# Kernel optimization log

Measured on AMD Instinct MI355X. Metric: run time of the kernel, lower is better.

The kernel has to match this reference:

```python
import jax, jax.numpy as jnp
import numpy as np

B, C, T, F = 4, 96, 320, 256
BN_EPS = 1e-5


def _cbp(x, W, b, gamma, beta, mean, var, a):
    """1x1 Conv2d + BatchNorm2d (inference stats) + PReLU (single param)."""
    y = jnp.einsum('oc,bctf->botf', W, x) + b[None, :, None, None]
    scale = gamma * jax.lax.rsqrt(var + BN_EPS)
    y = (y - mean[None, :, None, None]) * scale[None, :, None, None] + beta[None, :, None, None]
    return jnp.where(y >= 0, y, a * y)


def setup_inputs() -> dict:
    key = jax.random.key(0)
    ks = jax.random.split(key, 24)
    d = {"inp": jax.random.normal(ks[0], (B, C, T, F), dtype=jnp.float32)}

    def mk_params(i, cout):
        kk = jax.random.split(ks[i], 7)
        return dict(
            W=jax.random.normal(kk[0], (cout, C), dtype=jnp.float32) / np.sqrt(C),
            b=jnp.zeros((cout,), dtype=jnp.float32),
            gamma=jnp.ones((cout,), dtype=jnp.float32) + 0.1 * jax.random.normal(kk[1], (cout,), dtype=jnp.float32),
            beta=0.1 * jax.random.normal(kk[2], (cout,), dtype=jnp.float32),
            mean=0.1 * jax.random.normal(kk[3], (cout,), dtype=jnp.float32),
            var=jax.random.uniform(kk[4], (cout,), dtype=jnp.float32) + 0.5,
            a=jnp.float32(0.25),
        )

    for tag, i, cout in (("f", 1, 3 * C), ("t", 2, 2 * C), ("p", 3, C)):
        p = mk_params(i, cout)
        for k, v in p.items():
            d[k + "_" + tag] = v
    return d


def reference(inp,
              W_f, b_f, gamma_f, beta_f, mean_f, var_f, a_f,
              W_t, b_t, gamma_t, beta_t, mean_t, var_t, a_t,
              W_p, b_p, gamma_p, beta_p, mean_p, var_p, a_p):
    c = inp.shape[1]
    scale = 1.0 / jnp.sqrt(jnp.float32(c))

    # frequency-axis attention
    f_qkv = _cbp(inp, W_f, b_f, gamma_f, beta_f, mean_f, var_f, a_f)  # [B,3C,T,F]
    qf, kf, v = f_qkv[:, :c], f_qkv[:, c:2 * c], f_qkv[:, 2 * c:]
    f_score = jnp.einsum('bctf,bcty->btfy', qf, kf) * scale
    f_score = jax.nn.softmax(f_score, axis=-1)
    f_out = jnp.einsum('btfy,bcty->bctf', f_score, v)

    # time-axis attention (NOTE: original's masked_fill is non-inplace and
    # its result is discarded, so the causal mask has NO effect; replicated.)
    t_qk = _cbp(inp, W_t, b_t, gamma_t, beta_t, mean_t, var_t, a_t)  # [B,2C,T,F]
    qt, kt = t_qk[:, :c], t_qk[:, c:]
    t_score = jnp.einsum('bctf,bcyf->bfty', qt, kt) * scale
    t_score = jax.nn.softmax(t_score, axis=-1)
    t_out = jnp.einsum('bfty,bcyf->bctf', t_score, f_out)

    out = _cbp(t_out, W_p, b_p, gamma_p, beta_p, mean_p, var_p, a_p)
    return out + inp
```

## Files before the change

kernel.cpp:

```cpp
#include <hip/hip_runtime.h>
#include <math.h>

typedef float f4 __attribute__((ext_vector_type(4)));
typedef float f2 __attribute__((ext_vector_type(2)));
typedef float f32x4 __attribute__((ext_vector_type(4)));
typedef _Float16 h8 __attribute__((ext_vector_type(8)));

constexpr int B_ = 4, C_ = 96, T_ = 320, F_ = 256;
constexpr int TF_ = T_ * F_;
constexpr float EPS_ = 1e-5f;
constexpr size_t QH_ = (size_t)C_ * TF_;

constexpr int WHF = 0, WLF = 27648, WHT = 55296, WLT = 73728,
              WHP = 92160, WLP = 101376, WTOT = 110592;

__global__ __launch_bounds__(256)
void prep_kernel(const float* __restrict__ Wf, const float* __restrict__ Wt,
                 const float* __restrict__ Wp,
                 const float* __restrict__ bf, const float* __restrict__ gf,
                 const float* __restrict__ bef, const float* __restrict__ mf,
                 const float* __restrict__ vf,
                 const float* __restrict__ bt, const float* __restrict__ gt,
                 const float* __restrict__ bet, const float* __restrict__ mt,
                 const float* __restrict__ vt,
                 const float* __restrict__ bp, const float* __restrict__ gp,
                 const float* __restrict__ bep, const float* __restrict__ mp,
                 const float* __restrict__ vp,
                 _Float16* __restrict__ wsp, float* __restrict__ scsh)
{
    const int gtid = blockIdx.x * 256 + threadIdx.x;
    const int gsz  = gridDim.x * 256;
    for (int i = gtid; i < 27648; i += gsz) {
        const float w = Wf[i]; const _Float16 h = (_Float16)w;
        wsp[WHF + i] = h; wsp[WLF + i] = (_Float16)(w - (float)h);
    }
    for (int i = gtid; i < 18432; i += gsz) {
        const float w = Wt[i]; const _Float16 h = (_Float16)w;
        wsp[WHT + i] = h; wsp[WLT + i] = (_Float16)(w - (float)h);
    }
    for (int i = gtid; i < 9216; i += gsz) {
        const float w = Wp[i]; const _Float16 h = (_Float16)w;
        wsp[WHP + i] = h; wsp[WLP + i] = (_Float16)(w - (float)h);
    }
    if (gtid < 288) {
        const float sc = gf[gtid] * rsqrtf(vf[gtid] + EPS_);
        scsh[2 * gtid] = sc;
        scsh[2 * gtid + 1] = fmaf(bf[gtid] - mf[gtid], sc, bef[gtid]);
    } else if (gtid < 480) {
        const int i = gtid - 288;
        const float sc = gt[i] * rsqrtf(vt[i] + EPS_);
        scsh[576 + 2 * i] = sc;
        scsh[576 + 2 * i + 1] = fmaf(bt[i] - mt[i], sc, bet[i]);
    } else if (gtid < 576) {
        const int i = gtid - 480;
        const float sc = gp[i] * rsqrtf(vp[i] + EPS_);
        scsh[960 + 2 * i] = sc;
        scsh[960 + 2 * i + 1] = fmaf(bp[i] - mp[i], sc, bep[i]);
    }
}

__global__ __launch_bounds__(256, 3)
void conv_ft(const float* __restrict__ x, const _Float16* __restrict__ wsp,
             const float* __restrict__ scsh,
             const float* __restrict__ aPf, const float* __restrict__ aPt,
             _Float16* __restrict__ yf, _Float16* __restrict__ yt,
             int bsx, int bsyf, int bsyt)
{
    constexpr int LS = 200;
    extern __shared__ _Float16 ldsh[];
    _Float16* Xs = ldsh;

    x  += (size_t)blockIdx.y * bsx;
    yf += (size_t)blockIdx.y * bsyf;
    yt += (size_t)blockIdx.y * bsyt;

    const int tid = threadIdx.x;
    const int p0  = blockIdx.x * 64;

    const float* xg = x + p0;
    for (int e = tid; e < 64 * 12; e += 256) {
        const int p = e & 63, k0 = (e >> 6) * 8;
        const float* xp = xg + (size_t)k0 * TF_ + p;
        h8 hv, lv;
#pragma unroll
        for (int j = 0; j < 8; ++j) {
            const float xv = xp[(size_t)j * TF_];
            const _Float16 xh = (_Float16)xv;
            hv[j] = xh;
            lv[j] = (_Float16)(xv - (float)xh);
        }
        *(h8*)&Xs[p * LS + k0]      = hv;
        *(h8*)&Xs[p * LS + 96 + k0] = lv;
    }

    const int lane = tid & 63, wid = tid >> 6;
    const int l16 = lane & 15, lg = lane >> 4;
    const int wm = wid >> 1, wn = wid & 1;
    const float af_ = aPf[0], at_ = aPt[0];
    __syncthreads();

#pragma unroll 1
    for (int cg = 0; cg < 5; ++cg) {
        const _Float16 *Wh, *Wl; const float* ss; float a; _Float16* yo;
        if (cg < 3) {
            Wh = wsp + WHF + cg * 9216;  Wl = wsp + WLF + cg * 9216;
            ss = scsh + cg * 192;        a = af_;
            yo = yf + (size_t)cg * QH_;
        } else {
            const int c2 = cg - 3;
            Wh = wsp + WHT + c2 * 9216;  Wl = wsp + WLT + c2 * 9216;
            ss = scsh + 576 + c2 * 192;  a = at_;
            yo = yt + (size_t)c2 * QH_;
        }

        f32x4 acc[3][2];
#pragma unroll
        for (int m = 0; m < 3; ++m)
#pragma unroll
            for (int n = 0; n < 2; ++n) acc[m][n] = (f32x4){0.f, 0.f, 0.f, 0.f};

#pragma unroll
        for (int kk = 0; kk < 3; ++kk) {
            h8 bfh[2], bfl[2];
#pragma unroll
            for (int n = 0; n < 2; ++n) {
                const int prow = (wn * 2 + n) * 16 + l16;
                bfh[n] = *(const h8*)&Xs[prow * LS + kk * 32 + lg * 8];
                bfl[n] = *(const h8*)&Xs[prow * LS + 96 + kk * 32 + lg * 8];
            }
#pragma unroll
            for (int m = 0; m < 3; ++m) {
                const int row = (wm * 3 + m) * 16 + l16;
                const h8 wh = *(const h8*)&Wh[row * 96 + kk * 32 + lg * 8];
                const h8 wl = *(const h8*)&Wl[row * 96 + kk * 32 + lg * 8];
#pragma unroll
                for (int n = 0; n < 2; ++n) {
                    acc[m][n] = __builtin_amdgcn_mfma_f32_16x16x32_f16(wh, bfh[n], acc[m][n], 0, 0, 0);
                    acc[m][n] = __builtin_amdgcn_mfma_f32_16x16x32_f16(wl, bfh[n], acc[m][n], 0, 0, 0);
                    acc[m][n] = __builtin_amdgcn_mfma_f32_16x16x32_f16(wh, bfl[n], acc[m][n], 0, 0, 0);
                }
            }
        }

#pragma unroll
        for (int m = 0; m < 3; ++m) {
#pragma unroll
            for (int r = 0; r < 4; ++r) {
                const int col = (wm * 3 + m) * 16 + lg * 4 + r;
                const f2 sp = *(const f2*)&ss[2 * col];
                _Float16* yr = yo + (size_t)col * TF_ + p0 + wn * 32 + l16;
#pragma unroll
                for (int n = 0; n < 2; ++n) {
                    const float v = fmaf(acc[m][n][r], sp[0], sp[1]);
                    yr[n * 16] = (_Float16)(v >= 0.f ? v : a * v);
                }
            }
        }
    }
}

__global__ __launch_bounds__(256, 3)
void conv_p(const _Float16* __restrict__ x, const _Float16* __restrict__ wsp,
            const float* __restrict__ scsh, const float* __restrict__ aPp,
            _Float16* __restrict__ y, int bsx, int bsy)
{
    constexpr int LS = 104, PT = 160, NN = 5;
    extern __shared__ _Float16 ldsh[];
    _Float16* Xs = ldsh;

    x += (size_t)blockIdx.y * bsx;
    y += (size_t)blockIdx.y * bsy;

    const int tid = threadIdx.x;
    const int pt  = blockIdx.x & 1;
    const int g   = blockIdx.x >> 1;
    const int p0  = pt * PT;

    const _Float16* xg = x + (size_t)g * 96 * T_ + p0;
    for (int e = tid; e < PT * 12; e += 256) {
        const int p = e % PT, k0 = (e / PT) * 8;
        const _Float16* xp = xg + (size_t)k0 * T_ + p;
        h8 hv;
#pragma unroll
        for (int j = 0; j < 8; ++j) hv[j] = xp[(size_t)j * T_];
        *(h8*)&Xs[p * LS + k0] = hv;
    }

    const int lane = tid & 63, wid = tid >> 6;
    const int l16 = lane & 15, lg = lane >> 4;
    const int wm = wid >> 1, wn = wid & 1;
    const float a = aPp[0];
    const _Float16* Wh = wsp + WHP;
    const _Float16* Wl = wsp + WLP;
    const float* ss = scsh + 960;
    __syncthreads();

    f32x4 acc[3][NN];
#pragma unroll
    for (int m = 0; m < 3; ++m)
#pragma unroll
        for (int n = 0; n < NN; ++n) acc[m][n] = (f32x4){0.f, 0.f, 0.f, 0.f};

#pragma unroll
    for (int kk = 0; kk < 3; ++kk) {
        h8 bf[NN];
#pragma unroll
        for (int n = 0; n < NN; ++n)
            bf[n] = *(const h8*)&Xs[((wn * NN + n) * 16 + l16) * LS + kk * 32 + lg * 8];
#pragma unroll
        for (int m = 0; m < 3; ++m) {
            const int row = (wm * 3 + m) * 16 + l16;
            const h8 wh = *(const h8*)&Wh[row * 96 + kk * 32 + lg * 8];
            const h8 wl = *(const h8*)&Wl[row * 96 + kk * 32 + lg * 8];
#pragma unroll
            for (int n = 0; n < NN; ++n) {
                acc[m][n] = __builtin_amdgcn_mfma_f32_16x16x32_f16(wh, bf[n], acc[m][n], 0, 0, 0);
                acc[m][n] = __builtin_amdgcn_mfma_f32_16x16x32_f16(wl, bf[n], acc[m][n], 0, 0, 0);
            }
        }
    }

#pragma unroll
    for (int m = 0; m < 3; ++m) {
#pragma unroll
        for (int r = 0; r < 4; ++r) {
            const int col = (wm * 3 + m) * 16 + lg * 4 + r;
            const f2 sp = *(const f2*)&ss[2 * col];
            _Float16* yr = y + ((size_t)g * 96 + col) * T_ + p0 + wn * NN * 16 + l16;
#pragma unroll
            for (int n = 0; n < NN; ++n) {
                const float v = fmaf(acc[m][n][r], sp[0], sp[1]);
                yr[n * 16] = (_Float16)(v >= 0.f ? v : a * v);
            }
        }
    }
}

__device__ __forceinline__ void tr64_body(const _Float16* __restrict__ in,
                                          _Float16* __restrict__ out,
                                          int Mo, int No, int n0, int m0,
                                          _Float16* tile)
{
    const int t = threadIdx.x, ty = t >> 3, tx8 = t & 7;
#pragma unroll
    for (int r = 0; r < 2; ++r) {
        const int n = ty + r * 32;
        const h8 v = *(const h8*)&in[(size_t)(n0 + n) * Mo + m0 + tx8 * 8];
        const int c = tx8 ^ (n >> 3);
        *(h8*)&tile[n * 72 + c * 8] = v;
    }
    __syncthreads();
#pragma unroll
    for (int r = 0; r < 2; ++r) {
        const int mt = ty + r * 32;
        h8 v;
#pragma unroll
        for (int j = 0; j < 8; ++j) {
            const int n = tx8 * 8 + j;
            const int c = (mt >> 3) ^ tx8;
            v[j] = tile[n * 72 + c * 8 + (mt & 7)];
        }
        *(h8*)&out[(size_t)(m0 + mt) * No + n0 + tx8 * 8] = v;
    }
}

__global__ __launch_bounds__(256)
void transpose_trA(const _Float16* __restrict__ doh, _Float16* __restrict__ wsh)
{
    __shared__ _Float16 tile[64 * 72];
    const int b = blockIdx.z >> 1, t = blockIdx.z & 1;
    const _Float16* in  = t ? doh + (size_t)b * 2 * QH_
                            : wsh + (size_t)b * 3 * QH_;
    _Float16*       out = t ? wsh + (size_t)b * 3 * QH_ + 2 * QH_
                            : wsh + (size_t)b * 3 * QH_ + QH_;
    tr64_body(in, out, F_, C_ * T_, blockIdx.x * 64, blockIdx.y * 64, tile);
}

__global__ __launch_bounds__(256)
void transpose_trB(const _Float16* __restrict__ doh, _Float16* __restrict__ wsh)
{
    __shared__ _Float16 tile[64 * 72];
    const int b = blockIdx.z;
    tr64_body(doh + (size_t)b * 2 * QH_ + QH_, wsh + (size_t)b * 3 * QH_,
              F_, C_ * T_, blockIdx.x * 64, blockIdx.y * 64, tile);
}

__global__ __launch_bounds__(256)
void transpose_hf_res(const _Float16* __restrict__ in, const float* __restrict__ res,
                      float* __restrict__ out, int si, int sr, int so)
{
    __shared__ _Float16 tile[64 * 72];
    in  += (size_t)blockIdx.z * si;
    res += (size_t)blockIdx.z * sr;
    out += (size_t)blockIdx.z * so;
    const int n0 = blockIdx.x * 64, m0 = blockIdx.y * 64;
    const int t = threadIdx.x, ty = t >> 3, tx8 = t & 7;
#pragma unroll
    for (int r = 0; r < 2; ++r) {
        const int n = ty + r * 32;
        const h8 v = *(const h8*)&in[(size_t)(n0 + n) * (C_ * T_) + m0 + tx8 * 8];
        const int c = tx8 ^ (n >> 3);
        *(h8*)&tile[n * 72 + c * 8] = v;
    }
    __syncthreads();
#pragma unroll
    for (int r = 0; r < 2; ++r) {
        const int mt = ty + r * 32;
        const size_t obase = (size_t)(m0 + mt) * F_ + n0 + tx8 * 8;
        const f4 r0 = *(const f4*)&res[obase];
        const f4 r1 = *(const f4*)&res[obase + 4];
        f4 o0, o1;
#pragma unroll
        for (int j = 0; j < 8; ++j) {
            const int n = tx8 * 8 + j;
            const int c = (mt >> 3) ^ tx8;
            const float v = (float)tile[n * 72 + c * 8 + (mt & 7)];
            if (j < 4) o0[j] = v + r0[j]; else o1[j - 4] = v + r1[j - 4];
        }
        *(f4*)&out[obase]     = o0;
        *(f4*)&out[obase + 4] = o1;
    }
}

template<int MODE>
__global__ __launch_bounds__(256, 2)
void attn_mfma(const _Float16* __restrict__ Qb, const _Float16* __restrict__ Kb,
               const _Float16* __restrict__ Vb, _Float16* __restrict__ Ob,
               int qs, int ks, int vs, int os)
{
    constexpr int NY  = (MODE == 0) ? 256 : 320;
    constexpr int LD  = (MODE == 0) ? TF_ : T_;
    constexpr int NT  = NY / 16;
    constexpr int NYK = NY / 32;
    constexpr int KS  = 104;
    constexpr int VPS = NY + 24;
    constexpr int KVH = (NY * KS > 96 * VPS) ? NY * KS : 96 * VPS;
    constexpr int NG  = (MODE == 0) ? T_ : F_;
    constexpr int GOFF = (MODE == 0) ? F_ : C_ * T_;

    extern __shared__ _Float16 ldsh[];
    _Float16* KV = ldsh;
    _Float16* Pw = ldsh + KVH;

    const int lb    = blockIdx.y;
    const int strip = blockIdx.x / NG;
    const int grp   = blockIdx.x % NG;
    const int m0    = strip * 64;
    const size_t off = (size_t)grp * GOFF;
    const _Float16* Q = Qb + (size_t)lb * qs + off;
    const _Float16* K = Kb + (size_t)lb * ks + off;
    const _Float16* V = Vb + (size_t)lb * vs + off;
    _Float16*       O = Ob + (size_t)lb * os + off;

    const int tid  = threadIdx.x;
    const int lane = tid & 63, wid = tid >> 6;
    const int l16  = lane & 15, lg = lane >> 4;
    const int mw   = wid * 16;
    const float scale = 0.10206207261596575f;

    for (int e = tid; e < NY * 12; e += 256) {
        const int yy = e % NY, k0 = (e / NY) * 8;
        const _Float16* kp = K + (size_t)k0 * LD + yy;
        h8 hv;
#pragma unroll
        for (int j = 0; j < 8; ++j) hv[j] = kp[(size_t)j * LD];
        *(h8*)&KV[yy * KS + k0] = hv;
    }

    h8 aQ[3];
#pragma unroll
    for (int kk = 0; kk < 3; ++kk) {
        const _Float16* qp = Q + (size_t)(kk * 32 + lg * 8) * LD + m0 + mw + l16;
#pragma unroll
        for (int j = 0; j < 8; ++j) aQ[kk][j] = qp[(size_t)j * LD];
    }
    __syncthreads();

    f32x4 sacc[NT];
#pragma unroll
    for (int t = 0; t < NT; ++t) sacc[t] = (f32x4){0.f, 0.f, 0.f, 0.f};
#pragma unroll
    for (int kk = 0; kk < 3; ++kk) {
#pragma unroll
        for (int t = 0; t < NT; ++t) {
            const h8 bK = *(const h8*)&KV[(t * 16 + l16) * KS + kk * 32 + lg * 8];
            sacc[t] = __builtin_amdgcn_mfma_f32_16x16x32_f16(aQ[kk], bK, sacc[t], 0, 0, 0);
        }
    }

#pragma unroll
    for (int r = 0; r < 4; ++r) {
        float mx = sacc[0][r];
#pragma unroll
        for (int t = 1; t < NT; ++t) mx = fmaxf(mx, sacc[t][r]);
        for (int d = 1; d < 16; d <<= 1) mx = fmaxf(mx, __shfl_xor(mx, d));
        float pv[NT];
        float sum = 0.f;
#pragma unroll
        for (int t = 0; t < NT; ++t) {
            pv[t] = __expf((sacc[t][r] - mx) * scale); sum += pv[t];
        }
        for (int d = 1; d < 16; d <<= 1) sum += __shfl_xor(sum, d);
        const float inv = 1.f / sum;
#pragma unroll
        for (int t = 0; t < NT; ++t) sacc[t][r] = pv[t] * inv;
    }
    __syncthreads();

    constexpr int NY8 = NY / 8;
    for (int e = tid; e < 96 * NY8; e += 256) {
        const int c = e / NY8, y8 = e - c * NY8;
        *(h8*)&KV[c * VPS + y8 * 8] = *(const h8*)(V + (size_t)c * LD + y8 * 8);
    }
    __syncthreads();

    _Float16* Pme = Pw + wid * 640;
    f32x4 oacc[6];
#pragma unroll
    for (int ct = 0; ct < 6; ++ct) oacc[ct] = (f32x4){0.f, 0.f, 0.f, 0.f};

#pragma unroll
    for (int yk = 0; yk < NYK; ++yk) {
#pragma unroll
        for (int h = 0; h < 2; ++h)
#pragma unroll
            for (int r = 0; r < 4; ++r)
                Pme[(lg * 4 + r) * 40 + h * 16 + l16] = (_Float16)sacc[2 * yk + h][r];
        const h8 pf = *(const h8*)&Pme[l16 * 40 + lg * 8];
#pragma unroll
        for (int ct = 0; ct < 6; ++ct) {
            const h8 av = *(const h8*)&KV[(ct * 16 + l16) * VPS + yk * 32 + lg * 8];
            oacc[ct] = __builtin_amdgcn_mfma_f32_16x16x32_f16(av, pf, oacc[ct], 0, 0, 0);
        }
    }
#pragma unroll
    for (int ct = 0; ct < 6; ++ct)
#pragma unroll
        for (int r = 0; r < 4; ++r)
            O[(size_t)(ct * 16 + lg * 4 + r) * LD + m0 + mw + l16] = (_Float16)oacc[ct][r];
}

extern "C" void kernel_launch(void* const* d_in, const int* in_sizes, int n_in,
                              void* d_out, int out_size, void* d_ws, size_t ws_size,
                              hipStream_t stream)
{
    const float* inp = (const float*)d_in[0];
    const float* W_f = (const float*)d_in[1];  const float* b_f = (const float*)d_in[2];
    const float* g_f = (const float*)d_in[3];  const float* be_f = (const float*)d_in[4];
    const float* m_f = (const float*)d_in[5];  const float* v_f = (const float*)d_in[6];
    const float* a_f = (const float*)d_in[7];
    const float* W_t = (const float*)d_in[8];  const float* b_t = (const float*)d_in[9];
    const float* g_t = (const float*)d_in[10]; const float* be_t = (const float*)d_in[11];
    const float* m_t = (const float*)d_in[12]; const float* v_t = (const float*)d_in[13];
    const float* a_t = (const float*)d_in[14];
    const float* W_p = (const float*)d_in[15]; const float* b_p = (const float*)d_in[16];
    const float* g_p = (const float*)d_in[17]; const float* be_p = (const float*)d_in[18];
    const float* m_p = (const float*)d_in[19]; const float* v_p = (const float*)d_in[20];
    const float* a_p = (const float*)d_in[21];

    hipFuncSetAttribute((const void*)conv_ft,
                        hipFuncAttributeMaxDynamicSharedMemorySize, 25600);
    hipFuncSetAttribute((const void*)conv_p,
                        hipFuncAttributeMaxDynamicSharedMemorySize, 33280);
    hipFuncSetAttribute((const void*)attn_mfma<0>,
                        hipFuncAttributeMaxDynamicSharedMemorySize, 58880);
    hipFuncSetAttribute((const void*)attn_mfma<1>,
                        hipFuncAttributeMaxDynamicSharedMemorySize, 71680);

    constexpr int QH = (int)QH_;
    const size_t need4 = (size_t)12 * QH * 2 + (size_t)WTOT * 2 + 1152 * 4 + 4096;
    const int G = (ws_size >= need4) ? 4 : 2;

    _Float16* wsh  = (_Float16*)d_ws;
    _Float16* wsp  = wsh + (size_t)3 * G * QH;
    float*    scsh = (float*)(wsp + WTOT);

    prep_kernel<<<dim3(128), dim3(256), 0, stream>>>(
        W_f, W_t, W_p, b_f, g_f, be_f, m_f, v_f,
        b_t, g_t, be_t, m_t, v_t, b_p, g_p, be_p, m_p, v_p, wsp, scsh);

    for (int p = 0; p < B_ / G; ++p) {
        const float* xb  = inp + (size_t)p * G * QH;
        float*       dob = (float*)d_out + (size_t)p * G * QH;
        _Float16*    doh = (_Float16*)dob;

        conv_ft<<<dim3(1280, G), dim3(256), 25600, stream>>>(
            xb, wsp, scsh, a_f, a_t, wsh, doh, QH, 3 * QH, 2 * QH);
        attn_mfma<0><<<dim3(T_ * (F_ / 64), G), dim3(256), 58880, stream>>>(
            wsh, wsh + QH_, wsh + 2 * QH_, wsh, 3 * QH, 3 * QH, 3 * QH, 3 * QH);
        transpose_trA<<<dim3(480, 4, 2 * G), dim3(256), 0, stream>>>(doh, wsh);
        transpose_trB<<<dim3(480, 4, G), dim3(256), 0, stream>>>(doh, wsh);
        attn_mfma<1><<<dim3(F_ * (T_ / 64), G), dim3(256), 71680, stream>>>(
            wsh + 2 * QH_, wsh, wsh + QH_, wsh + 2 * QH_,
            3 * QH, 3 * QH, 3 * QH, 3 * QH);
        conv_p<<<dim3(F_ * 2, G), dim3(256), 33280, stream>>>(
            wsh + 2 * QH_, wsp, scsh, a_p, wsh, 3 * QH, 3 * QH);
        transpose_hf_res<<<dim3(4, 480, G), dim3(256), 0, stream>>>(
            wsh, xb, dob, 3 * QH, QH, QH);
    }
}
```

Baseline: 724.4 us.

## Process two pixel tiles per conv_ft block with register prefetch of second tile

Each conv_ft block now handles two 64-pixel tiles instead of one. The second tile's fp32 input is loaded into registers before the first tile's MFMA work, then split to fp16 hi/lo into a second LDS buffer. The aim is to hide global-load latency behind compute and halve the block count. The cost is 24 extra live floats per thread and double the LDS per block, which may lower occupancy under launch_bounds(256,3).

```diff
diff --git a/kernel.cpp b/kernel.cpp
--- a/kernel.cpp
+++ b/kernel.cpp
@@ -68,29 +68,33 @@
 {
     constexpr int LS = 200;
     extern __shared__ _Float16 ldsh[];
-    _Float16* Xs = ldsh;
+    _Float16* Xs0 = ldsh;
+    _Float16* Xs1 = ldsh + 64 * LS;
 
     x  += (size_t)blockIdx.y * bsx;
     yf += (size_t)blockIdx.y * bsyf;
     yt += (size_t)blockIdx.y * bsyt;
 
     const int tid = threadIdx.x;
-    const int p0  = blockIdx.x * 64;
-
-    const float* xg = x + p0;
-    for (int e = tid; e < 64 * 12; e += 256) {
-        const int p = e & 63, k0 = (e >> 6) * 8;
-        const float* xp = xg + (size_t)k0 * TF_ + p;
-        h8 hv, lv;
-#pragma unroll
-        for (int j = 0; j < 8; ++j) {
-            const float xv = xp[(size_t)j * TF_];
-            const _Float16 xh = (_Float16)xv;
-            hv[j] = xh;
-            lv[j] = (_Float16)(xv - (float)xh);
-        }
-        *(h8*)&Xs[p * LS + k0]      = hv;
-        *(h8*)&Xs[p * LS + 96 + k0] = lv;
+    const int p0A = blockIdx.x * 128;
+    const int p0B = p0A + 64;
+
+    {
+        const float* xg = x + p0A;
+        for (int e = tid; e < 64 * 12; e += 256) {
+            const int p = e & 63, k0 = (e >> 6) * 8;
+            const float* xp = xg + (size_t)k0 * TF_ + p;
+            h8 hv, lv;
+#pragma unroll
+            for (int j = 0; j < 8; ++j) {
+                const float xv = xp[(size_t)j * TF_];
+                const _Float16 xh = (_Float16)xv;
+                hv[j] = xh;
+                lv[j] = (_Float16)(xv - (float)xh);
+            }
+            *(h8*)&Xs0[p * LS + k0]      = hv;
+            *(h8*)&Xs0[p * LS + 96 + k0] = lv;
+        }
     }
 
     const int lane = tid & 63, wid = tid >> 6;
@@ -99,64 +103,96 @@
     const float af_ = aPf[0], at_ = aPt[0];
     __syncthreads();
 
+    float xpre[3][8];
+#pragma unroll
+    for (int it = 0; it < 3; ++it) {
+        const int e = tid + it * 256;
+        const int p = e & 63, k0 = (e >> 6) * 8;
+        const float* xp = x + p0B + (size_t)k0 * TF_ + p;
+#pragma unroll
+        for (int j = 0; j < 8; ++j) xpre[it][j] = xp[(size_t)j * TF_];
+    }
+
+    auto compute5 = [&](const _Float16* Xs, int p0) {
 #pragma unroll 1
-    for (int cg = 0; cg < 5; ++cg) {
-        const _Float16 *Wh, *Wl; const float* ss; float a; _Float16* yo;
-        if (cg < 3) {
-            Wh = wsp + WHF + cg * 9216;  Wl = wsp + WLF + cg * 9216;
-            ss = scsh + cg * 192;        a = af_;
-            yo = yf + (size_t)cg * QH_;
-        } else {
-            const int c2 = cg - 3;
-            Wh = wsp + WHT + c2 * 9216;  Wl = wsp + WLT + c2 * 9216;
-            ss = scsh + 576 + c2 * 192;  a = at_;
-            yo = yt + (size_t)c2 * QH_;
-        }
-
-        f32x4 acc[3][2];
-#pragma unroll
-        for (int m = 0; m < 3; ++m)
-#pragma unroll
-            for (int n = 0; n < 2; ++n) acc[m][n] = (f32x4){0.f, 0.f, 0.f, 0.f};
-
-#pragma unroll
-        for (int kk = 0; kk < 3; ++kk) {
-            h8 bfh[2], bfl[2];
-#pragma unroll
-            for (int n = 0; n < 2; ++n) {
-                const int prow = (wn * 2 + n) * 16 + l16;
-                bfh[n] = *(const h8*)&Xs[prow * LS + kk * 32 + lg * 8];
-                bfl[n] = *(const h8*)&Xs[prow * LS + 96 + kk * 32 + lg * 8];
+        for (int cg = 0; cg < 5; ++cg) {
+            const _Float16 *Wh, *Wl; const float* ss; float a; _Float16* yo;
+            if (cg < 3) {
+                Wh = wsp + WHF + cg * 9216;  Wl = wsp + WLF + cg * 9216;
+                ss = scsh + cg * 192;        a = af_;
+                yo = yf + (size_t)cg * QH_;
+            } else {
+                const int c2 = cg - 3;
+                Wh = wsp + WHT + c2 * 9216;  Wl = wsp + WLT + c2 * 9216;
+                ss = scsh + 576 + c2 * 192;  a = at_;
+                yo = yt + (size_t)c2 * QH_;
             }
-#pragma unroll
-            for (int m = 0; m < 3; ++m) {
-                const int row = (wm * 3 + m) * 16 + l16;
-                const h8 wh = *(const h8*)&Wh[row * 96 + kk * 32 + lg * 8];
-                const h8 wl = *(const h8*)&Wl[row * 96 + kk * 32 + lg * 8];
+
+            f32x4 acc[3][2];
+#pragma unroll
+            for (int m = 0; m < 3; ++m)
+#pragma unroll
+                for (int n = 0; n < 2; ++n) acc[m][n] = (f32x4){0.f, 0.f, 0.f, 0.f};
+
+#pragma unroll
+            for (int kk = 0; kk < 3; ++kk) {
+                h8 bfh[2], bfl[2];
 #pragma unroll
                 for (int n = 0; n < 2; ++n) {
-                    acc[m][n] = __builtin_amdgcn_mfma_f32_16x16x32_f16(wh, bfh[n], acc[m][n], 0, 0, 0);
-                    acc[m][n] = __builtin_amdgcn_mfma_f32_16x16x32_f16(wl, bfh[n], acc[m][n], 0, 0, 0);
-                    acc[m][n] = __builtin_amdgcn_mfma_f32_16x16x32_f16(wh, bfl[n], acc[m][n], 0, 0, 0);
+                    const int prow = (wn * 2 + n) * 16 + l16;
+                    bfh[n] = *(const h8*)&Xs[prow * LS + kk * 32 + lg * 8];
+                    bfl[n] = *(const h8*)&Xs[prow * LS + 96 + kk * 32 + lg * 8];
+                }
+#pragma unroll
+                for (int m = 0; m < 3; ++m) {
+                    const int row = (wm * 3 + m) * 16 + l16;
+                    const h8 wh = *(const h8*)&Wh[row * 96 + kk * 32 + lg * 8];
+                    const h8 wl = *(const h8*)&Wl[row * 96 + kk * 32 + lg * 8];
+#pragma unroll
+                    for (int n = 0; n < 2; ++n) {
+                        acc[m][n] = __builtin_amdgcn_mfma_f32_16x16x32_f16(wh, bfh[n], acc[m][n], 0, 0, 0);
+                        acc[m][n] = __builtin_amdgcn_mfma_f32_16x16x32_f16(wl, bfh[n], acc[m][n], 0, 0, 0);
+                        acc[m][n] = __builtin_amdgcn_mfma_f32_16x16x32_f16(wh, bfl[n], acc[m][n], 0, 0, 0);
+                    }
                 }
             }
-        }
-
-#pragma unroll
-        for (int m = 0; m < 3; ++m) {
-#pragma unroll
-            for (int r = 0; r < 4; ++r) {
-                const int col = (wm * 3 + m) * 16 + lg * 4 + r;
-                const f2 sp = *(const f2*)&ss[2 * col];
-                _Float16* yr = yo + (size_t)col * TF_ + p0 + wn * 32 + l16;
-#pragma unroll
-                for (int n = 0; n < 2; ++n) {
-                    const float v = fmaf(acc[m][n][r], sp[0], sp[1]);
-                    yr[n * 16] = (_Float16)(v >= 0.f ? v : a * v);
+
+#pragma unroll
+            for (int m = 0; m < 3; ++m) {
+#pragma unroll
+                for (int r = 0; r < 4; ++r) {
+                    const int col = (wm * 3 + m) * 16 + lg * 4 + r;
+                    const f2 sp = *(const f2*)&ss[2 * col];
+                    _Float16* yr = yo + (size_t)col * TF_ + p0 + wn * 32 + l16;
+#pragma unroll
+                    for (int n = 0; n < 2; ++n) {
+                        const float v = fmaf(acc[m][n][r], sp[0], sp[1]);
+                        yr[n * 16] = (_Float16)(v >= 0.f ? v : a * v);
+                    }
                 }
             }
         }
-    }
+    };
+
+    compute5(Xs0, p0A);
+
+#pragma unroll
+    for (int it = 0; it < 3; ++it) {
+        const int e = tid + it * 256;
+        const int p = e & 63, k0 = (e >> 6) * 8;
+        h8 hv, lv;
+#pragma unroll
+        for (int j = 0; j < 8; ++j) {
+            const _Float16 xh = (_Float16)xpre[it][j];
+            hv[j] = xh;
+            lv[j] = (_Float16)(xpre[it][j] - (float)xh);
+        }
+        *(h8*)&Xs1[p * LS + k0]      = hv;
+        *(h8*)&Xs1[p * LS + 96 + k0] = lv;
+    }
+    __syncthreads();
+
+    compute5(Xs1, p0B);
 }
 
 __global__ __launch_bounds__(256, 3)
@@ -459,7 +495,7 @@
     const float* a_p = (const float*)d_in[21];
 
     hipFuncSetAttribute((const void*)conv_ft,
-                        hipFuncAttributeMaxDynamicSharedMemorySize, 25600);
+                        hipFuncAttributeMaxDynamicSharedMemorySize, 51200);
     hipFuncSetAttribute((const void*)conv_p,
                         hipFuncAttributeMaxDynamicSharedMemorySize, 33280);
     hipFuncSetAttribute((const void*)attn_mfma<0>,
@@ -484,7 +520,7 @@
         float*       dob = (float*)d_out + (size_t)p * G * QH;
         _Float16*    doh = (_Float16*)dob;
 
-        conv_ft<<<dim3(1280, G), dim3(256), 25600, stream>>>(
+        conv_ft<<<dim3(640, G), dim3(256), 51200, stream>>>(
             xb, wsp, scsh, a_f, a_t, wsh, doh, QH, 3 * QH, 2 * QH);
         attn_mfma<0><<<dim3(T_ * (F_ / 64), G), dim3(256), 58880, stream>>>(
             wsh, wsh + QH_, wsh + 2 * QH_, wsh, 3 * QH, 3 * QH, 3 * QH, 3 * QH);
```

After: 713.7 us. Within noise of the previous version (-1.5%).
